# Kernel optimization log

Measured on AMD Instinct MI355X. Metric: run time of the kernel, lower is better.

Reference implementation:

```python
import jax, jax.numpy as jnp
import numpy as np

L, V, D, S_MAX, B, S, H = 8, 32000, 1024, 1024, 4, 1024, 16
FF = 4 * D
EPS = 1e-5


def setup_inputs() -> dict:
    key = jax.random.key(0)
    ks = jax.random.split(key, 20)
    g = lambda k, shape: jax.random.normal(k, shape, dtype=jnp.float32) * 0.02
    inp = {
        'tokens': jax.random.randint(ks[0], (B, S), 0, V, dtype=jnp.int32),
        'num_heads': H,
        'emb': g(ks[1], (V, D)),
        'pos_emb': g(ks[2], (S_MAX, D)),
        'Wq': g(ks[3], (L, D, D)), 'bq': jnp.zeros((L, D), jnp.float32),
        'Wk': g(ks[4], (L, D, D)), 'bk': jnp.zeros((L, D), jnp.float32),
        'Wv': g(ks[5], (L, D, D)), 'bv': jnp.zeros((L, D), jnp.float32),
        'Wo': g(ks[6], (L, D, D)), 'bo': jnp.zeros((L, D), jnp.float32),
        'n1_s': jnp.ones((L, D), jnp.float32), 'n1_b': jnp.zeros((L, D), jnp.float32),
        'W1': g(ks[7], (L, D, FF)), 'b1': jnp.zeros((L, FF), jnp.float32),
        'W2': g(ks[8], (L, FF, D)), 'b2': jnp.zeros((L, D), jnp.float32),
        'n2_s': jnp.ones((L, D), jnp.float32), 'n2_b': jnp.zeros((L, D), jnp.float32),
    }
    return inp


def _layernorm(x, s, b):
    mu = jnp.mean(x, axis=-1, keepdims=True)
    var = jnp.mean(jnp.square(x - mu), axis=-1, keepdims=True)
    return s * (x - mu) * jax.lax.rsqrt(var + EPS) + b


def _forward(tokens, num_heads, emb, pos_emb, Wq, bq, Wk, bk, Wv, bv, Wo, bo,
             n1_s, n1_b, W1, b1, W2, b2, n2_s, n2_b):
    Bn, Sn = tokens.shape
    d = emb.shape[1]
    hd = d // num_heads
    x = emb[tokens] + pos_emb[:Sn][None, :, :]  # [B,S,D]

    def split_heads(t):  # [B,S,D] -> [B,H,S,hd]
        return t.reshape(Bn, Sn, num_heads, hd).transpose(0, 2, 1, 3)

    causal = jnp.triu(jnp.ones((Sn, Sn), dtype=bool), k=1)
    scale = 1.0 / np.sqrt(hd)
    nlayers = Wq.shape[0]
    for l in range(nlayers):
        q = split_heads(x @ Wq[l] + bq[l])
        k = split_heads(x @ Wk[l] + bk[l])
        v = split_heads(x @ Wv[l] + bv[l])
        scores = jnp.einsum('bhqd,bhkd->bhqk', q, k) * scale
        scores = jnp.where(causal, -jnp.inf, scores)
        attn = jax.nn.softmax(scores, axis=-1)
        ctx = jnp.einsum('bhqk,bhkd->bhqd', attn, v)
        ctx = ctx.transpose(0, 2, 1, 3).reshape(Bn, Sn, d)
        x = _layernorm(x + (ctx @ Wo[l] + bo[l]), n1_s[l], n1_b[l])
        h = jax.nn.relu(x @ W1[l] + b1[l])
        x = _layernorm(x + (h @ W2[l] + b2[l]), n2_s[l], n2_b[l])
    return x @ emb.T  # tied output head -> [B,S,V]


def reference(tokens, num_heads, emb, pos_emb, Wq, bq, Wk, bk, Wv, bv, Wo, bo,
              n1_s, n1_b, W1, b1, W2, b2, n2_s, n2_b):
    return _forward(tokens, num_heads, emb, pos_emb, Wq, bq, Wk, bk, Wv, bv,
                    Wo, bo, n1_s, n1_b, W1, b1, W2, b2, n2_s, n2_b)
```

## Files before the change

### kernel.cpp

```cpp
#include <hip/hip_runtime.h>

#define D_MODEL 1024
#define SEQ     1024
#define BATCH   4
#define NHEAD   16
#define HDIM    64
#define FF_DIM  4096
#define NLAYER  8
#define VOCAB   32000
#define ROWS    (BATCH*SEQ)
#define QKV_N   3072
#define LN_EPS  1e-5f

typedef __attribute__((ext_vector_type(4))) float   f32x4;
typedef __attribute__((ext_vector_type(8))) unsigned short u16x8;
typedef __attribute__((ext_vector_type(8))) __bf16  bf16x8;

typedef const unsigned int __attribute__((address_space(1)))* gas_t;
typedef unsigned int __attribute__((address_space(3)))* las_t;

__device__ __forceinline__ void gld16(const void* g, void* l) {
    __builtin_amdgcn_global_load_lds((gas_t)g, (las_t)l, 16, 0, 0);
}

__device__ __forceinline__ unsigned short f2bf(float f) {
    unsigned int u = __builtin_bit_cast(unsigned int, f);
    u += 0x7FFFu + ((u >> 16) & 1u);
    return (unsigned short)(u >> 16);
}

__device__ __forceinline__ float bf2f(unsigned short u) {
    return __builtin_bit_cast(float, (unsigned int)u << 16);
}

__device__ __forceinline__ f32x4 mfma32(u16x8 a, u16x8 b, f32x4 c) {
    return __builtin_amdgcn_mfma_f32_16x16x32_bf16(
        __builtin_bit_cast(bf16x8, a), __builtin_bit_cast(bf16x8, b), c, 0, 0, 0);
}

__global__ __launch_bounds__(256) void embed_k(
    const int* __restrict__ tok, const float* __restrict__ emb,
    const float* __restrict__ pos, unsigned short* __restrict__ xb)
{
    int bs = blockIdx.x;
    int s  = bs & (SEQ - 1);
    int tk = tok[bs];
    int c  = threadIdx.x * 4;
    float4 e = *(const float4*)(emb + (size_t)tk * D_MODEL + c);
    float4 p = *(const float4*)(pos + (size_t)s * D_MODEL + c);
    float y0 = e.x + p.x, y1 = e.y + p.y, y2 = e.z + p.z, y3 = e.w + p.w;
    size_t base = (size_t)bs * D_MODEL + c;
    unsigned long long pk = (unsigned long long)f2bf(y0)
        | ((unsigned long long)f2bf(y1) << 16)
        | ((unsigned long long)f2bf(y2) << 32)
        | ((unsigned long long)f2bf(y3) << 48);
    *(unsigned long long*)(xb + base) = pk;
}

__global__ __launch_bounds__(256) void cast_bf(
    const float* __restrict__ in, unsigned short* __restrict__ out, size_t n)
{
    size_t i = ((size_t)blockIdx.x * 256 + threadIdx.x) * 4;
    if (i >= n) return;
    float4 v = *(const float4*)(in + i);
    unsigned long long pk = (unsigned long long)f2bf(v.x)
        | ((unsigned long long)f2bf(v.y) << 16)
        | ((unsigned long long)f2bf(v.z) << 32)
        | ((unsigned long long)f2bf(v.w) << 48);
    *(unsigned long long*)(out + i) = pk;
}

__global__ __launch_bounds__(256) void bias3_k(
    const float* __restrict__ bq, const float* __restrict__ bk,
    const float* __restrict__ bv, float* __restrict__ out)
{
    int l = blockIdx.x / 3, which = blockIdx.x % 3;
    const float* src = which == 0 ? bq : (which == 1 ? bk : bv);
    int i = threadIdx.x * 4;
    float4 v = *(const float4*)(src + (size_t)l * D_MODEL + i);
    *(float4*)(out + (size_t)l * QKV_N + which * D_MODEL + i) = v;
}

__device__ __forceinline__ void tc_tile(
    const float* __restrict__ W, unsigned short* __restrict__ Wt,
    int K, int N, int n0, int k0)
{
    __shared__ float t[64][65];
    int rr = threadIdx.x >> 4;
    int cc = (threadIdx.x & 15) * 4;
#pragma unroll
    for (int it = 0; it < 4; it++) {
        int r = it * 16 + rr;
        float4 v = *(const float4*)(W + (size_t)(k0 + r) * N + n0 + cc);
        t[r][cc] = v.x; t[r][cc + 1] = v.y; t[r][cc + 2] = v.z; t[r][cc + 3] = v.w;
    }
    __syncthreads();
#pragma unroll
    for (int it = 0; it < 4; it++) {
        int n = it * 16 + rr;
        unsigned long long pk = (unsigned long long)f2bf(t[cc][n])
            | ((unsigned long long)f2bf(t[cc + 1][n]) << 16)
            | ((unsigned long long)f2bf(t[cc + 2][n]) << 32)
            | ((unsigned long long)f2bf(t[cc + 3][n]) << 48);
        *(unsigned long long*)(Wt + (size_t)(n0 + n) * K + k0 + cc) = pk;
    }
}

__global__ __launch_bounds__(256) void transpose_cast(
    const float* __restrict__ W, unsigned short* __restrict__ Wt, int K, int N)
{
    tc_tile(W, Wt, K, N, blockIdx.x * 64, blockIdx.y * 64);
}

__global__ __launch_bounds__(256) void transpose_cast3(
    const float* __restrict__ Wq, const float* __restrict__ Wk,
    const float* __restrict__ Wv, unsigned short* __restrict__ Wt)
{
    const int which = blockIdx.z;
    const float* W = which == 0 ? Wq : (which == 1 ? Wk : Wv);
    tc_tile(W, Wt + (size_t)which * (1024 * 1024), 1024, 1024,
            blockIdx.x * 64, blockIdx.y * 64);
}

__global__ __launch_bounds__(256) void transpose_all(
    const float* __restrict__ Wq, const float* __restrict__ Wk,
    const float* __restrict__ Wv, const float* __restrict__ Wo,
    const float* __restrict__ W1, const float* __restrict__ W2,
    unsigned short* __restrict__ wt)
{
    int b = blockIdx.x;
    const float* W; unsigned short* out; int K, N, t;
    if (b < 768)       { int w = b >> 8; t = b & 255; W = w == 0 ? Wq : (w == 1 ? Wk : Wv);
                         out = wt + (size_t)w * 1048576; K = 1024; N = 1024; }
    else if (b < 1024) { t = b - 768;  W = Wo; out = wt + (size_t)3 * 1048576; K = 1024; N = 1024; }
    else if (b < 2048) { t = b - 1024; W = W1; out = wt + (size_t)4 * 1048576; K = 1024; N = 4096; }
    else               { t = b - 2048; W = W2; out = wt + (size_t)8 * 1048576; K = 4096; N = 1024; }
    int ntx = N >> 6;
    tc_tile(W, out, K, N, (t % ntx) * 64, (t / ntx) * 64);
}

template<int MODE>
__global__ __launch_bounds__(256, 3) void gemm_bt(
    const unsigned short* __restrict__ A, int lda,
    const unsigned short* __restrict__ Bt, int ldb,
    const float* __restrict__ bias, void* __restrict__ Cout, int N, int Klen)
{
    __shared__ unsigned short As[128 * 32];
    __shared__ unsigned short Bs[128 * 32];
    const int part = blockIdx.y;
    A  += (size_t)part * Klen;
    Bt += (size_t)part * Klen;
    int flat = blockIdx.x;
    const int bm = flat & 31, bn = flat >> 5;
    const int tid  = threadIdx.x;
    const int wid  = tid >> 6, lane = tid & 63;
    const int l16  = lane & 15, lhi = lane >> 4;
    const int wr   = wid >> 1, wc = wid & 1;

    const int srow = wid * 32 + (lane >> 2);
    const int scol = (lane & 3) * 8;
    const unsigned short* gA0 = A  + ((size_t)bm * 128 + srow) * lda + scol;
    const unsigned short* gB0 = Bt + ((size_t)bn * 128 + srow) * ldb + scol;
    unsigned short* lA = As + wid * 32 * 32;
    unsigned short* lB = Bs + wid * 32 * 32;

    f32x4 acc[4][4];
#pragma unroll
    for (int i = 0; i < 4; i++)
#pragma unroll
        for (int j = 0; j < 4; j++) acc[i][j] = (f32x4){0.f, 0.f, 0.f, 0.f};

    for (int k0 = 0; k0 < Klen; k0 += 32) {
        __syncthreads();
        gld16(gA0 + k0,                    lA);
        gld16(gA0 + k0 + 16 * (size_t)lda, lA + 16 * 32);
        gld16(gB0 + k0,                    lB);
        gld16(gB0 + k0 + 16 * (size_t)ldb, lB + 16 * 32);
        __syncthreads();
        u16x8 af[4], bfr[4];
#pragma unroll
        for (int i = 0; i < 4; i++)
            af[i] = *(const u16x8*)(As + (wr * 64 + i * 16 + l16) * 32 + lhi * 8);
#pragma unroll
        for (int i = 0; i < 4; i++)
            bfr[i] = *(const u16x8*)(Bs + (wc * 64 + i * 16 + l16) * 32 + lhi * 8);
#pragma unroll
        for (int mi = 0; mi < 4; mi++)
#pragma unroll
            for (int ni = 0; ni < 4; ni++)
                acc[mi][ni] = mfma32(af[mi], bfr[ni], acc[mi][ni]);
    }

    const size_t pofs = (size_t)part * (size_t)ROWS * N;
#pragma unroll
    for (int mi = 0; mi < 4; mi++) {
        float bv[4];
#pragma unroll
        for (int ni = 0; ni < 4; ni++)
            bv[ni] = (bias && part == 0) ? bias[bn * 128 + wc * 64 + ni * 16 + l16] : 0.f;
#pragma unroll
        for (int j = 0; j < 4; j++) {
            int row = bm * 128 + wr * 64 + mi * 16 + lhi * 4 + j;
#pragma unroll
            for (int ni = 0; ni < 4; ni++) {
                int col = bn * 128 + wc * 64 + ni * 16 + l16;
                float v = acc[mi][ni][j] + bv[ni];
                size_t idx = pofs + (size_t)row * N + col;
                if constexpr (MODE == 1) {
                    ((unsigned short*)Cout)[idx] = f2bf(v);
                } else {
                    ((unsigned short*)Cout)[idx] = f2bf(v > 0.f ? v : 0.f);
                }
            }
        }
    }
}

#define PSYNC() do { __builtin_amdgcn_s_barrier(); \
    asm volatile("s_waitcnt lgkmcnt(0)" ::: "memory"); \
    __builtin_amdgcn_sched_barrier(0); } while (0)
#define PEND() __builtin_amdgcn_s_barrier()
#define VM4()  asm volatile("s_waitcnt vmcnt(4)" ::: "memory")

#define LOADA(reg, half) do { \
    _Pragma("unroll") \
    for (int m_ = 0; m_ < 4; m_++) { \
        aF[m_][0] = *(const u16x8*)((reg) + ((half)*4 + m_) * 2048 + lane0); \
        aF[m_][1] = *(const u16x8*)((reg) + ((half)*4 + m_) * 2048 + lane1); \
    } } while (0)

#define LOADB(reg, np) do { \
    _Pragma("unroll") \
    for (int n_ = 0; n_ < 2; n_++) { \
        bF[(np)*2 + n_][0] = *(const u16x8*)((reg) + ((np)*2 + n_) * 2048 + lane0); \
        bF[(np)*2 + n_][1] = *(const u16x8*)((reg) + ((np)*2 + n_) * 2048 + lane1); \
    } } while (0)

#define MFMA8(ma, np) do { \
    __builtin_amdgcn_s_setprio(1); \
    _Pragma("unroll") \
    for (int m_ = 0; m_ < 4; m_++) \
        _Pragma("unroll") \
        for (int n_ = 0; n_ < 2; n_++) { \
            acc[(ma)+m_][(np)*2+n_] = mfma32(aF[m_][0], bF[(np)*2+n_][0], acc[(ma)+m_][(np)*2+n_]); \
            acc[(ma)+m_][(np)*2+n_] = mfma32(aF[m_][1], bF[(np)*2+n_][1], acc[(ma)+m_][(np)*2+n_]); \
        } \
    __builtin_amdgcn_s_setprio(0); \
} while (0)

template<int MODE, int SWZ>
__global__ __launch_bounds__(512, 2) void gemm256(
    const unsigned short* __restrict__ A, const unsigned short* __restrict__ Bt,
    const float* __restrict__ bias, void* __restrict__ Cout, int N, int K)
{
    __shared__ unsigned short lds[65536] __attribute__((aligned(128)));
    const int tid = threadIdx.x, wid = tid >> 6, lane = tid & 63;
    const int l16 = lane & 15, lhi = lane >> 4;
    const int wr = wid >> 2, wc = wid & 3;

    int flat = blockIdx.x;
    if constexpr (SWZ) {
        int cpx = gridDim.x >> 3; flat = (flat & 7) * cpx + (flat >> 3);
    }
    const int bm = flat & 15, bn = flat >> 4;
    const int NT = K >> 6;

    const int srowL = tid >> 3;
    const int scolb = ((tid & 7) << 4) ^ (((tid >> 3) & 7) << 4);
    const unsigned short* baseA = A  + (size_t)(bm * 256 + srowL) * K + (scolb >> 1);
    const unsigned short* baseB = Bt + (size_t)(bn * 256 + srowL) * K + (scolb >> 1);
    unsigned short* dst0 = lds + wid * 512;

    auto stage = [&](int isB, int tile, int h) {
        const unsigned short* s = (isB ? baseB : baseA) + (size_t)(h * 128) * K + (size_t)tile * 64;
        unsigned short* d = dst0 + (tile & 1) * 32768 + isB * 16384 + h * 8192;
        gld16(s, d);
        gld16(s + (size_t)64 * K, d + 4096);
    };

    const int lswz  = (l16 & 7) << 4;
    const int lane0 = ((lhi * 16) ^ lswz) + l16 * 128;
    const int lane1 = ((64 + lhi * 16) ^ lswz) + l16 * 128;

    const char* aR0 = (const char*)lds + wr * 16384;
    const char* bR0 = (const char*)lds + 32768 + (wc >> 1) * 16384 + (wc & 1) * 8192;
    const char* aR1 = aR0 + 65536;
    const char* bR1 = bR0 + 65536;

    f32x4 acc[8][4];
#pragma unroll
    for (int i = 0; i < 8; i++)
#pragma unroll
        for (int j = 0; j < 4; j++) acc[i][j] = (f32x4){0.f, 0.f, 0.f, 0.f};
    u16x8 aF[4][2], bF[4][2];

    stage(1, 0, 0); stage(1, 0, 1);
    stage(0, 0, 0); stage(0, 0, 1);
    stage(1, 1, 0); stage(1, 1, 1);
    VM4();
    __builtin_amdgcn_s_barrier();

    for (int t = 0; t < NT; t += 2) {
        const bool more = (t + 2) < NT;
        LOADA(aR0, 0); LOADB(bR0, 0); stage(0, t + 1, 0);
        PSYNC(); MFMA8(0, 0); PEND();
        LOADB(bR0, 1);                stage(0, t + 1, 1);
        PSYNC(); MFMA8(0, 1); PEND();
        LOADA(aR0, 1);                if (more) stage(1, t + 2, 0);
        PSYNC(); MFMA8(4, 0); PEND();
        if (more) { stage(1, t + 2, 1); VM4(); }
        else      { asm volatile("s_waitcnt vmcnt(0)" ::: "memory"); }
        PSYNC(); MFMA8(4, 1); PEND();
        LOADA(aR1, 0); LOADB(bR1, 0); if (more) stage(0, t + 2, 0);
        PSYNC(); MFMA8(0, 0); PEND();
        LOADB(bR1, 1);                if (more) stage(0, t + 2, 1);
        PSYNC(); MFMA8(0, 1); PEND();
        LOADA(aR1, 1);                if (more) stage(1, t + 3, 0);
        PSYNC(); MFMA8(4, 0); PEND();
        if (more) { stage(1, t + 3, 1); VM4(); }
        PSYNC(); MFMA8(4, 1); PEND();
    }

#pragma unroll
    for (int mi = 0; mi < 8; mi++) {
        float bv[4];
#pragma unroll
        for (int ni = 0; ni < 4; ni++)
            bv[ni] = bias ? bias[bn * 256 + wc * 64 + ni * 16 + l16] : 0.f;
#pragma unroll
        for (int j = 0; j < 4; j++) {
            int row = bm * 256 + wr * 128 + mi * 16 + lhi * 4 + j;
#pragma unroll
            for (int ni = 0; ni < 4; ni++) {
                int col = bn * 256 + wc * 64 + ni * 16 + l16;
                float v = acc[mi][ni][j] + bv[ni];
                size_t idx = (size_t)row * N + col;
                if constexpr (MODE == 0) {
                    __builtin_nontemporal_store(v, (float*)Cout + idx);
                } else if constexpr (MODE == 1) {
                    ((unsigned short*)Cout)[idx] = f2bf(v);
                } else {
                    ((unsigned short*)Cout)[idx] = f2bf(v > 0.f ? v : 0.f);
                }
            }
        }
    }
}

__global__ __launch_bounds__(256, 3) void attn_fwd(
    const unsigned short* __restrict__ qkv, unsigned short* __restrict__ ctxb)
{
    __shared__ unsigned short Ks[64 * 72];
    __shared__ unsigned short Vs[64 * 72];
    __shared__ unsigned short Ps[4 * 16 * 72];
    const int tid = threadIdx.x;
    const int wid = tid >> 6, lane = tid & 63;
    const int l16 = lane & 15, lhi = lane >> 4;
    const int bh  = blockIdx.y, b = bh >> 4, h = bh & 15;
    const int p   = blockIdx.x;
    const int qA0 = p * 64;
    const int qB0 = (15 - p) * 64;
    const size_t rowbase = (size_t)b * SEQ;

    const unsigned short* qpA = qkv + (rowbase + qA0 + wid * 16 + l16) * QKV_N + h * HDIM + lhi * 8;
    u16x8 qAf0 = *(const u16x8*)qpA;
    u16x8 qAf1 = *(const u16x8*)(qpA + 32);
    const unsigned short* qpB = qkv + (rowbase + qB0 + wid * 16 + l16) * QKV_N + h * HDIM + lhi * 8;
    u16x8 qBf0 = *(const u16x8*)qpB;
    u16x8 qBf1 = *(const u16x8*)(qpB + 32);

    f32x4 oaA[4], oaB[4];
    float mjA[4], ljA[4], mjB[4], ljB[4];
#pragma unroll
    for (int i = 0; i < 4; i++) {
        oaA[i] = (f32x4){0.f, 0.f, 0.f, 0.f};
        oaB[i] = (f32x4){0.f, 0.f, 0.f, 0.f};
        mjA[i] = -1e30f; ljA[i] = 0.f;
        mjB[i] = -1e30f; ljB[i] = 0.f;
    }

    auto update = [&](u16x8 qf0, u16x8 qf1, f32x4 (&oa)[4],
                      float (&mj)[4], float (&lj)[4], int q0, int kv0) {
        f32x4 sa[4];
        __builtin_amdgcn_s_setprio(1);
#pragma unroll
        for (int ni = 0; ni < 4; ni++) {
            f32x4 z = (f32x4){0.f, 0.f, 0.f, 0.f};
            u16x8 k0f = *(const u16x8*)(&Ks[(ni * 16 + l16) * 72 + lhi * 8]);
            u16x8 k1f = *(const u16x8*)(&Ks[(ni * 16 + l16) * 72 + 32 + lhi * 8]);
            z = mfma32(qf0, k0f, z);
            z = mfma32(qf1, k1f, z);
            sa[ni] = z;
        }
        __builtin_amdgcn_s_setprio(0);
        float tm[4] = {-1e30f, -1e30f, -1e30f, -1e30f};
#pragma unroll
        for (int ni = 0; ni < 4; ni++)
#pragma unroll
            for (int j = 0; j < 4; j++) {
                float v = sa[ni][j] * 0.125f;
                int row = q0 + wid * 16 + lhi * 4 + j;
                int col = kv0 + ni * 16 + l16;
                if (col > row) v = -1e30f;
                sa[ni][j] = v;
                tm[j] = fmaxf(tm[j], v);
            }
#pragma unroll
        for (int j = 0; j < 4; j++) {
#pragma unroll
            for (int off = 1; off < 16; off <<= 1)
                tm[j] = fmaxf(tm[j], __shfl_xor(tm[j], off));
        }
        float al[4], rs[4] = {0.f, 0.f, 0.f, 0.f};
#pragma unroll
        for (int j = 0; j < 4; j++) {
            float mn = fmaxf(mj[j], tm[j]);
            al[j] = __expf(mj[j] - mn);
            mj[j] = mn;
        }
#pragma unroll
        for (int ni = 0; ni < 4; ni++)
#pragma unroll
            for (int j = 0; j < 4; j++) {
                float pv = __expf(sa[ni][j] - mj[j]);
                rs[j] += pv;
                Ps[wid * 1152 + (lhi * 4 + j) * 72 + ni * 16 + l16] = f2bf(pv);
            }
#pragma unroll
        for (int j = 0; j < 4; j++) {
#pragma unroll
            for (int off = 1; off < 16; off <<= 1)
                rs[j] += __shfl_xor(rs[j], off);
            lj[j] = lj[j] * al[j] + rs[j];
        }
#pragma unroll
        for (int di = 0; di < 4; di++)
#pragma unroll
            for (int j = 0; j < 4; j++) oa[di][j] *= al[j];
        __builtin_amdgcn_s_setprio(1);
#pragma unroll
        for (int di = 0; di < 4; di++) {
#pragma unroll
            for (int kc = 0; kc < 2; kc++) {
                u16x8 pf = *(const u16x8*)(&Ps[wid * 1152 + l16 * 72 + kc * 32 + lhi * 8]);
                u16x8 vf = *(const u16x8*)(&Vs[(di * 16 + l16) * 72 + kc * 32 + lhi * 8]);
                oa[di] = mfma32(pf, vf, oa[di]);
            }
        }
        __builtin_amdgcn_s_setprio(0);
    };

    const int ntB = 16 - p;
    for (int kt = 0; kt < ntB; ++kt) {
        const int kv0 = kt * 64;
        __syncthreads();
#pragma unroll
        for (int it = 0; it < 2; ++it) {
            int e = it * 256 + tid;
            int r = e >> 3, d0 = (e & 7) * 8;
            size_t goff = (rowbase + kv0 + r) * QKV_N + D_MODEL + h * HDIM + d0;
            u16x8 kk = *(const u16x8*)(qkv + goff);
            *(u16x8*)(&Ks[r * 72 + d0]) = kk;
        }
        if (tid < 128) {
            int r0 = (tid & 15) * 4, d0v = (tid >> 4) * 8;
            const unsigned short* vp = qkv + (rowbase + kv0 + r0) * QKV_N
                                       + 2 * D_MODEL + h * HDIM + d0v;
            u16x8 w0 = *(const u16x8*)vp;
            u16x8 w1 = *(const u16x8*)(vp + QKV_N);
            u16x8 w2 = *(const u16x8*)(vp + 2 * QKV_N);
            u16x8 w3 = *(const u16x8*)(vp + 3 * QKV_N);
#pragma unroll
            for (int j = 0; j < 8; j++) {
                unsigned long long pk = (unsigned long long)w0[j]
                    | ((unsigned long long)w1[j] << 16)
                    | ((unsigned long long)w2[j] << 32)
                    | ((unsigned long long)w3[j] << 48);
                *(unsigned long long*)(&Vs[(d0v + j) * 72 + r0]) = pk;
            }
        }
        __syncthreads();

        if (kt <= p) update(qAf0, qAf1, oaA, mjA, ljA, qA0, kv0);
        update(qBf0, qBf1, oaB, mjB, ljB, qB0, kv0);
    }

#pragma unroll
    for (int di = 0; di < 4; di++)
#pragma unroll
        for (int j = 0; j < 4; j++) {
            int rowA = qA0 + wid * 16 + lhi * 4 + j;
            ctxb[(rowbase + rowA) * D_MODEL + h * HDIM + di * 16 + l16] =
                f2bf(oaA[di][j] / ljA[j]);
            int rowB = qB0 + wid * 16 + lhi * 4 + j;
            ctxb[(rowbase + rowB) * D_MODEL + h * HDIM + di * 16 + l16] =
                f2bf(oaB[di][j] / ljB[j]);
        }
}

__global__ __launch_bounds__(256) void ln3(
    unsigned short* __restrict__ xb, const unsigned short* __restrict__ p0,
    const unsigned short* __restrict__ p1,
    const float* __restrict__ sc, const float* __restrict__ bi)
{
    const int row = blockIdx.x;
    const int t = threadIdx.x;
    const size_t base = (size_t)row * D_MODEL + t * 4;
    ushort4 xu = *(const ushort4*)(xb + base);
    ushort4 au = *(const ushort4*)(p0 + base);
    ushort4 bu = *(const ushort4*)(p1 + base);
    float v0 = bf2f(xu.x) + bf2f(au.x) + bf2f(bu.x);
    float v1 = bf2f(xu.y) + bf2f(au.y) + bf2f(bu.y);
    float v2 = bf2f(xu.z) + bf2f(au.z) + bf2f(bu.z);
    float v3 = bf2f(xu.w) + bf2f(au.w) + bf2f(bu.w);
    float sum = v0 + v1 + v2 + v3;
    float sq  = v0 * v0 + v1 * v1 + v2 * v2 + v3 * v3;
#pragma unroll
    for (int off = 1; off < 64; off <<= 1) {
        sum += __shfl_xor(sum, off);
        sq  += __shfl_xor(sq, off);
    }
    __shared__ float red[8];
    int wid = t >> 6, lane = t & 63;
    if (lane == 0) { red[wid] = sum; red[4 + wid] = sq; }
    __syncthreads();
    sum = red[0] + red[1] + red[2] + red[3];
    sq  = red[4] + red[5] + red[6] + red[7];
    float mu   = sum * (1.f / D_MODEL);
    float var  = sq * (1.f / D_MODEL) - mu * mu;
    float rstd = rsqrtf(var + LN_EPS);
    int c = t * 4;
    float4 sv = *(const float4*)(sc + c);
    float4 bv = *(const float4*)(bi + c);
    float y0 = sv.x * (v0 - mu) * rstd + bv.x;
    float y1 = sv.y * (v1 - mu) * rstd + bv.y;
    float y2 = sv.z * (v2 - mu) * rstd + bv.z;
    float y3 = sv.w * (v3 - mu) * rstd + bv.w;
    unsigned long long pk = (unsigned long long)f2bf(y0)
        | ((unsigned long long)f2bf(y1) << 16)
        | ((unsigned long long)f2bf(y2) << 32)
        | ((unsigned long long)f2bf(y3) << 48);
    *(unsigned long long*)(xb + base) = pk;
}

extern "C" void kernel_launch(void* const* d_in, const int* in_sizes, int n_in,
                              void* d_out, int out_size, void* d_ws, size_t ws_size,
                              hipStream_t stream)
{
    (void)in_sizes; (void)n_in; (void)out_size;
    const int*   tokens = (const int*)d_in[0];
    const float* emb  = (const float*)d_in[2];
    const float* pose = (const float*)d_in[3];
    const float* Wq = (const float*)d_in[4];
    const float* bq = (const float*)d_in[5];
    const float* Wk = (const float*)d_in[6];
    const float* bk = (const float*)d_in[7];
    const float* Wv = (const float*)d_in[8];
    const float* bv = (const float*)d_in[9];
    const float* Wo = (const float*)d_in[10];
    const float* bo = (const float*)d_in[11];
    const float* n1s = (const float*)d_in[12];
    const float* n1b = (const float*)d_in[13];
    const float* W1 = (const float*)d_in[14];
    const float* b1 = (const float*)d_in[15];
    const float* W2 = (const float*)d_in[16];
    const float* b2 = (const float*)d_in[17];
    const float* n2s = (const float*)d_in[18];
    const float* n2b = (const float*)d_in[19];

    char* w = (char*)d_ws;
    size_t off = 0;
    auto carve = [&](size_t bytes) -> void* {
        void* p = w + off;
        off = (off + bytes + 255) & ~(size_t)255;
        return p;
    };
    unsigned short* tmp = (unsigned short*)carve((size_t)2 * ROWS * D_MODEL * 2);
    unsigned short* xb    = (unsigned short*)carve((size_t)ROWS * D_MODEL * 2);
    unsigned short* qkvb  = (unsigned short*)carve((size_t)ROWS * QKV_N * 2);
    unsigned short* cbuf  = (unsigned short*)carve((size_t)ROWS * D_MODEL * 2);
    unsigned short* hbuf  = (unsigned short*)carve((size_t)ROWS * FF_DIM * 2);
    size_t wt_off = off;
    unsigned short* wt = (unsigned short*)carve((size_t)12 * 1048576 * 2);
    float* bqkv = (float*)carve((size_t)NLAYER * QKV_N * 4);
    unsigned short* embb = qkvb;
    unsigned short* tmp1 = tmp + (size_t)ROWS * D_MODEL;
    const bool fused_t = (off <= ws_size);
    if (!fused_t) {
        off = wt_off;
        wt = (unsigned short*)carve((size_t)D_MODEL * FF_DIM * 2);
        bqkv = (float*)carve((size_t)NLAYER * QKV_N * 4);
        if (off > ws_size) return;
    }

    bias3_k<<<NLAYER * 3, 256, 0, stream>>>(bq, bk, bv, bqkv);
    embed_k<<<ROWS, 256, 0, stream>>>(tokens, emb, pose, xb);

    for (int l = 0; l < NLAYER; l++) {
        const float* Wq_l = Wq + (size_t)l * D_MODEL * D_MODEL;
        const float* Wk_l = Wk + (size_t)l * D_MODEL * D_MODEL;
        const float* Wv_l = Wv + (size_t)l * D_MODEL * D_MODEL;
        const float* Wo_l = Wo + (size_t)l * D_MODEL * D_MODEL;
        const float* W1_l = W1 + (size_t)l * D_MODEL * FF_DIM;
        const float* W2_l = W2 + (size_t)l * FF_DIM * D_MODEL;

        unsigned short* wtQKV = wt;
        unsigned short* wtWo  = fused_t ? wt + (size_t)3 * 1048576 : wt;
        unsigned short* wtW1  = fused_t ? wt + (size_t)4 * 1048576 : wt;
        unsigned short* wtW2  = fused_t ? wt + (size_t)8 * 1048576 : wt;

        if (fused_t) {
            transpose_all<<<3072, 256, 0, stream>>>(Wq_l, Wk_l, Wv_l, Wo_l, W1_l, W2_l, wt);
        } else {
            transpose_cast3<<<dim3(16, 16, 3), 256, 0, stream>>>(Wq_l, Wk_l, Wv_l, wtQKV);
        }
        gemm_bt<1><<<dim3(768, 1), 256, 0, stream>>>(xb, D_MODEL, wtQKV, D_MODEL,
                                                     bqkv + (size_t)l * QKV_N, qkvb, QKV_N, D_MODEL);

        attn_fwd<<<dim3(8, BATCH * NHEAD), 256, 0, stream>>>(qkvb, cbuf);

        if (!fused_t) transpose_cast<<<dim3(16, 16), 256, 0, stream>>>(Wo_l, wtWo, D_MODEL, D_MODEL);
        gemm_bt<1><<<dim3(256, 2), 256, 0, stream>>>(cbuf, D_MODEL, wtWo, D_MODEL,
                                                     bo + (size_t)l * D_MODEL, tmp, D_MODEL, D_MODEL / 2);
        ln3<<<ROWS, 256, 0, stream>>>(xb, tmp, tmp1, n1s + (size_t)l * D_MODEL, n1b + (size_t)l * D_MODEL);

        if (!fused_t) transpose_cast<<<dim3(64, 16), 256, 0, stream>>>(W1_l, wtW1, D_MODEL, FF_DIM);
        gemm256<2, 1><<<(FF_DIM / 256) * 16, 512, 0, stream>>>(xb, wtW1, b1 + (size_t)l * FF_DIM, hbuf, FF_DIM, D_MODEL);
        if (!fused_t) transpose_cast<<<dim3(16, 64), 256, 0, stream>>>(W2_l, wtW2, FF_DIM, D_MODEL);
        gemm_bt<1><<<dim3(256, 2), 256, 0, stream>>>(hbuf, FF_DIM, wtW2, FF_DIM,
                                                     b2 + (size_t)l * D_MODEL, tmp, D_MODEL, FF_DIM / 2);
        ln3<<<ROWS, 256, 0, stream>>>(xb, tmp, tmp1, n2s + (size_t)l * D_MODEL, n2b + (size_t)l * D_MODEL);
    }

    cast_bf<<<(VOCAB * D_MODEL) / 1024, 256, 0, stream>>>(emb, embb, (size_t)VOCAB * D_MODEL);
    gemm256<0, 0><<<(VOCAB / 256) * 16, 512, 0, stream>>>(xb, embb, nullptr, d_out, VOCAB, D_MODEL);
}
```

Baseline: 2.058 ms.

## Transpose all layer weights in one launch and use 256-tile GEMM for QKV

Hoists the per-layer weight transpose/cast into a single kernel covering all eight layers, writing every layer's bf16 transposed weights to a larger workspace region. This removes seven kernel launches and lets the transpose run as one wide grid instead of eight smaller ones. The QKV projection also switches from the 128-tile gemm_bt to the 256-tile gemm256 kernel. The trade-off is a workspace of about 200 MB for weights; if the workspace is too small, it falls back to the old per-layer transpose.

```diff
diff --git a/kernel.cpp b/kernel.cpp
--- a/kernel.cpp
+++ b/kernel.cpp
@@ -135,6 +135,29 @@
     else if (b < 1024) { t = b - 768;  W = Wo; out = wt + (size_t)3 * 1048576; K = 1024; N = 1024; }
     else if (b < 2048) { t = b - 1024; W = W1; out = wt + (size_t)4 * 1048576; K = 1024; N = 4096; }
     else               { t = b - 2048; W = W2; out = wt + (size_t)8 * 1048576; K = 4096; N = 1024; }
+    int ntx = N >> 6;
+    tc_tile(W, out, K, N, (t % ntx) * 64, (t / ntx) * 64);
+}
+
+__global__ __launch_bounds__(256) void transpose_all_L(
+    const float* __restrict__ Wq, const float* __restrict__ Wk,
+    const float* __restrict__ Wv, const float* __restrict__ Wo,
+    const float* __restrict__ W1, const float* __restrict__ W2,
+    unsigned short* __restrict__ wtall)
+{
+    int b = blockIdx.x;
+    const int l = b / 3072;
+    b -= l * 3072;
+    const size_t sq = (size_t)l * 1048576;
+    const size_t sr = (size_t)l * 4194304;
+    unsigned short* wt = wtall + (size_t)l * (12 * 1048576);
+    const float* W; unsigned short* out; int K, N, t;
+    if (b < 768)       { int w = b >> 8; t = b & 255;
+                         W = (w == 0 ? Wq : (w == 1 ? Wk : Wv)) + sq;
+                         out = wt + (size_t)w * 1048576; K = 1024; N = 1024; }
+    else if (b < 1024) { t = b - 768;  W = Wo + sq; out = wt + (size_t)3 * 1048576; K = 1024; N = 1024; }
+    else if (b < 2048) { t = b - 1024; W = W1 + sr; out = wt + (size_t)4 * 1048576; K = 1024; N = 4096; }
+    else               { t = b - 2048; W = W2 + sr; out = wt + (size_t)8 * 1048576; K = 4096; N = 1024; }
     int ntx = N >> 6;
     tc_tile(W, out, K, N, (t % ntx) * 64, (t / ntx) * 64);
 }
@@ -580,53 +603,48 @@
     unsigned short* qkvb  = (unsigned short*)carve((size_t)ROWS * QKV_N * 2);
     unsigned short* cbuf  = (unsigned short*)carve((size_t)ROWS * D_MODEL * 2);
     unsigned short* hbuf  = (unsigned short*)carve((size_t)ROWS * FF_DIM * 2);
-    size_t wt_off = off;
-    unsigned short* wt = (unsigned short*)carve((size_t)12 * 1048576 * 2);
     float* bqkv = (float*)carve((size_t)NLAYER * QKV_N * 4);
     unsigned short* embb = qkvb;
     unsigned short* tmp1 = tmp + (size_t)ROWS * D_MODEL;
-    const bool fused_t = (off <= ws_size);
-    if (!fused_t) {
-        off = wt_off;
-        wt = (unsigned short*)carve((size_t)D_MODEL * FF_DIM * 2);
-        bqkv = (float*)carve((size_t)NLAYER * QKV_N * 4);
+
+    size_t big_off = off;
+    unsigned short* wtall = (unsigned short*)carve((size_t)NLAYER * 12 * 1048576 * 2);
+    bool all_t = (off <= ws_size);
+    unsigned short* wt = nullptr;
+    if (!all_t) {
+        off = big_off;
+        wt = (unsigned short*)carve((size_t)12 * 1048576 * 2);
         if (off > ws_size) return;
     }
 
     bias3_k<<<NLAYER * 3, 256, 0, stream>>>(bq, bk, bv, bqkv);
     embed_k<<<ROWS, 256, 0, stream>>>(tokens, emb, pose, xb);
+    if (all_t)
+        transpose_all_L<<<NLAYER * 3072, 256, 0, stream>>>(Wq, Wk, Wv, Wo, W1, W2, wtall);
 
     for (int l = 0; l < NLAYER; l++) {
-        const float* Wq_l = Wq + (size_t)l * D_MODEL * D_MODEL;
-        const float* Wk_l = Wk + (size_t)l * D_MODEL * D_MODEL;
-        const float* Wv_l = Wv + (size_t)l * D_MODEL * D_MODEL;
-        const float* Wo_l = Wo + (size_t)l * D_MODEL * D_MODEL;
-        const float* W1_l = W1 + (size_t)l * D_MODEL * FF_DIM;
-        const float* W2_l = W2 + (size_t)l * FF_DIM * D_MODEL;
-
-        unsigned short* wtQKV = wt;
-        unsigned short* wtWo  = fused_t ? wt + (size_t)3 * 1048576 : wt;
-        unsigned short* wtW1  = fused_t ? wt + (size_t)4 * 1048576 : wt;
-        unsigned short* wtW2  = fused_t ? wt + (size_t)8 * 1048576 : wt;
-
-        if (fused_t) {
-            transpose_all<<<3072, 256, 0, stream>>>(Wq_l, Wk_l, Wv_l, Wo_l, W1_l, W2_l, wt);
-        } else {
-            transpose_cast3<<<dim3(16, 16, 3), 256, 0, stream>>>(Wq_l, Wk_l, Wv_l, wtQKV);
-        }
-        gemm_bt<1><<<dim3(768, 1), 256, 0, stream>>>(xb, D_MODEL, wtQKV, D_MODEL,
-                                                     bqkv + (size_t)l * QKV_N, qkvb, QKV_N, D_MODEL);
+        unsigned short* wl = all_t ? wtall + (size_t)l * (12 * 1048576) : wt;
+        unsigned short* wtQKV = wl;
+        unsigned short* wtWo  = wl + (size_t)3 * 1048576;
+        unsigned short* wtW1  = wl + (size_t)4 * 1048576;
+        unsigned short* wtW2  = wl + (size_t)8 * 1048576;
+
+        if (!all_t) {
+            transpose_all<<<3072, 256, 0, stream>>>(
+                Wq + (size_t)l * D_MODEL * D_MODEL, Wk + (size_t)l * D_MODEL * D_MODEL,
+                Wv + (size_t)l * D_MODEL * D_MODEL, Wo + (size_t)l * D_MODEL * D_MODEL,
+                W1 + (size_t)l * D_MODEL * FF_DIM,  W2 + (size_t)l * FF_DIM * D_MODEL, wt);
+        }
+        gemm256<1, 1><<<(QKV_N / 256) * 16, 512, 0, stream>>>(xb, wtQKV,
+            bqkv + (size_t)l * QKV_N, qkvb, QKV_N, D_MODEL);
 
         attn_fwd<<<dim3(8, BATCH * NHEAD), 256, 0, stream>>>(qkvb, cbuf);
 
-        if (!fused_t) transpose_cast<<<dim3(16, 16), 256, 0, stream>>>(Wo_l, wtWo, D_MODEL, D_MODEL);
         gemm_bt<1><<<dim3(256, 2), 256, 0, stream>>>(cbuf, D_MODEL, wtWo, D_MODEL,
                                                      bo + (size_t)l * D_MODEL, tmp, D_MODEL, D_MODEL / 2);
         ln3<<<ROWS, 256, 0, stream>>>(xb, tmp, tmp1, n1s + (size_t)l * D_MODEL, n1b + (size_t)l * D_MODEL);
 
-        if (!fused_t) transpose_cast<<<dim3(64, 16), 256, 0, stream>>>(W1_l, wtW1, D_MODEL, FF_DIM);
         gemm256<2, 1><<<(FF_DIM / 256) * 16, 512, 0, stream>>>(xb, wtW1, b1 + (size_t)l * FF_DIM, hbuf, FF_DIM, D_MODEL);
-        if (!fused_t) transpose_cast<<<dim3(16, 64), 256, 0, stream>>>(W2_l, wtW2, FF_DIM, D_MODEL);
         gemm_bt<1><<<dim3(256, 2), 256, 0, stream>>>(hbuf, FF_DIM, wtW2, FF_DIM,
                                                      b2 + (size_t)l * D_MODEL, tmp, D_MODEL, FF_DIM / 2);
         ln3<<<ROWS, 256, 0, stream>>>(xb, tmp, tmp1, n2s + (size_t)l * D_MODEL, n2b + (size_t)l * D_MODEL);
```

New measurement: 2.128 ms. 3.4% more time.
